# Optimization experiments

Hardware: AMD Instinct MI355X
Metric: run time of the kernel (lower is better)

## Reference

```python
import jax, jax.numpy as jnp
import numpy as np

BN_EPS = 1e-5
LN_EPS = 1e-5


def setup_inputs() -> dict:
    key = jax.random.key(0)
    ks = jax.random.split(key, 8)
    B, D, T = 16, 96, 512  # batch, enc_in (channels), d_model (time/feature)
    H = 2 * T
    residual = jax.random.normal(ks[0], (B, D, T), dtype=jnp.float32)
    # BatchNorm1d(enc_in) affine params
    bn_gamma = jnp.ones((D,), dtype=jnp.float32)
    bn_beta = jnp.zeros((D,), dtype=jnp.float32)
    # LayerNorm(d_model) affine params
    ln_gamma = jnp.ones((T,), dtype=jnp.float32)
    ln_beta = jnp.zeros((T,), dtype=jnp.float32)
    # MLP: Linear(T, 2T) -> GELU -> Linear(2T, T)
    W1 = jax.random.normal(ks[1], (T, H), dtype=jnp.float32) / np.float32(np.sqrt(T))
    b1 = jnp.zeros((H,), dtype=jnp.float32)
    W2 = jax.random.normal(ks[2], (H, T), dtype=jnp.float32) / np.float32(np.sqrt(H))
    b2 = jnp.zeros((T,), dtype=jnp.float32)
    return {"residual": residual, "bn_gamma": bn_gamma, "bn_beta": bn_beta,
            "ln_gamma": ln_gamma, "ln_beta": ln_beta,
            "W1": W1, "b1": b1, "W2": W2, "b2": b2}


def _var_cor_attention(x):
    # x: [B, D, T]; queries = keys = values = x
    B, D, T = x.shape
    f = jnp.fft.rfft(x, axis=-1)                       # [B, D, F]
    # pairwise spectral product q_i * conj(k_j): [B, D, D, F]
    res = f[:, :, None, :] * jnp.conj(f[:, None, :, :])
    corr = jnp.fft.irfft(res, axis=-1).mean(axis=-1)   # [B, D, D]
    scale = np.float32(1.0 / np.sqrt(T))
    corr = jax.nn.softmax(corr * scale, axis=-1)
    V = jnp.einsum('bsd,bde->bse', corr, x)            # [B, D, T]
    return V


def reference(residual, bn_gamma, bn_beta, ln_gamma, ln_beta, W1, b1, W2, b2):
    # attention + residual
    x = _var_cor_attention(residual) + residual        # [B, D, T]
    # BatchNorm1d over channel dim D: stats over (B, T), biased variance
    mu = x.mean(axis=(0, 2), keepdims=True)
    var = ((x - mu) ** 2).mean(axis=(0, 2), keepdims=True)
    x = (x - mu) * jax.lax.rsqrt(var + BN_EPS)
    x = x * bn_gamma[None, :, None] + bn_beta[None, :, None]
    # MLP (exact GELU, torch default) + residual
    h = jax.nn.gelu(jnp.einsum('bdt,th->bdh', x, W1) + b1, approximate=False)
    y = jnp.einsum('bdh,ht->bdt', h, W2) + b2 + x
    # LayerNorm over last dim T
    mu2 = y.mean(axis=-1, keepdims=True)
    var2 = ((y - mu2) ** 2).mean(axis=-1, keepdims=True)
    y = (y - mu2) * jax.lax.rsqrt(var2 + LN_EPS)
    return y * ln_gamma + ln_beta
```

## Files before the change

kernel.cpp:

```cpp
#include <hip/hip_runtime.h>
#include <math.h>
#include <stdint.h>

#define BB 16
#define DD 96
#define TT 512
#define HH 1024
#define NROW (BB*DD)
#define KT2 (HH/32)

typedef __attribute__((ext_vector_type(4))) float floatx4;
typedef __attribute__((ext_vector_type(8))) short short8;

#define WSOFF_X     0u
#define WSOFF_HFRAG 3145728u
#define WSOFF_W1BF  6291456u
#define WSOFF_W2BF  7340032u
#define WSOFF_PS    8388608u
#define WSOFF_PS2   8437760u
#define WSOFF_S     8486912u

__device__ __forceinline__ uint16_t f2bf(float v) {
    uint32_t u = __float_as_uint(v);
    uint32_t r = 0x7fffu + ((u >> 16) & 1u);
    return (uint16_t)((u + r) >> 16);
}

__global__ __launch_bounds__(256) void k_pre(const float* __restrict__ residual,
                                             const float* __restrict__ W1,
                                             const float* __restrict__ W2,
                                             float* __restrict__ s,
                                             uint16_t* __restrict__ w1bf,
                                             uint16_t* __restrict__ w2bf) {
    const int bid = blockIdx.x;
    const int tid = threadIdx.x;
    const int wave = tid >> 6;
    const int lane = tid & 63;
    const int q = lane >> 4, l15 = lane & 15;

    if (bid < 96) {
        int row0 = bid*16 + wave*4;
        float acc[4] = {0.f, 0.f, 0.f, 0.f};
        #pragma unroll
        for (int cc = 0; cc < 4; ++cc) {
            const float* p = residual + (size_t)(row0 + cc)*TT;
            #pragma unroll
            for (int u = 0; u < TT/64; ++u) acc[cc] += p[lane + u*64];
        }
        #pragma unroll
        for (int o = 32; o > 0; o >>= 1) {
            #pragma unroll
            for (int cc = 0; cc < 4; ++cc) acc[cc] += __shfl_down(acc[cc], o, 64);
        }
        if (lane == 0) {
            #pragma unroll
            for (int cc = 0; cc < 4; ++cc) s[row0 + cc] = acc[cc];
        }
    } else {
        int wgid = (bid - 96)*4 + wave;
        const int nw = (512 - 96)*4;
        for (int u = wgid; u < 2048; u += nw) {
            const float* W; uint16_t* ob; int KT, N, b;
            if (u < 1024) { W = W1; ob = w1bf; KT = 16; N = 1024; b = u; }
            else          { W = W2; ob = w2bf; KT = 32; N = 512;  b = u - 1024; }
            int tile_n = b / KT, tile_k = b % KT;
            const float* src = W + (size_t)(tile_k*32 + q*8)*N + tile_n*16 + l15;
            uint16_t tmp[8];
            #pragma unroll
            for (int j = 0; j < 8; ++j) tmp[j] = f2bf(src[(size_t)j*N]);
            uint16_t* dst = ob + ((size_t)b*64 + lane)*8;
            *reinterpret_cast<ushort4*>(dst)     = *reinterpret_cast<ushort4*>(&tmp[0]);
            *reinterpret_cast<ushort4*>(dst + 4) = *reinterpret_cast<ushort4*>(&tmp[4]);
        }
    }
}

__global__ __launch_bounds__(256) void k_attn(const float* __restrict__ residual,
                                              const float* __restrict__ s,
                                              float* __restrict__ x,
                                              float* __restrict__ ps,
                                              float* __restrict__ ps2) {
    __shared__ float rlds[DD*64];
    __shared__ float slds[DD];
    __shared__ float aLDS[24*DD];
    const int u = blockIdx.x;
    const int b = u >> 5, chunk = (u >> 2) & 7, ig = u & 3;
    const int tid = threadIdx.x;
    const int wave = tid >> 6;
    const int lane = tid & 63;

    const float4* rb4 = reinterpret_cast<const float4*>(residual + (size_t)b*DD*TT);
    float4* rl4 = reinterpret_cast<float4*>(rlds);
    #pragma unroll
    for (int sx = 0; sx < 6; ++sx) {
        int idx = tid + sx*256;
        int i = idx >> 4, t4 = idx & 15;
        rl4[idx] = rb4[(size_t)i*(TT/4) + chunk*16 + t4];
    }
    if (tid < DD) slds[tid] = s[b*DD + tid];
    __syncthreads();

    const float c = 1.0f / (512.0f * 22.627416997969522f);
    float sj_lo = slds[lane];
    float sj_hi = (lane < 32) ? slds[64 + lane] : 0.f;
    #pragma unroll
    for (int rr = 0; rr < 6; ++rr) {
        int iloc = wave*6 + rr;
        float si = slds[ig*24 + iloc] * c;
        float v1 = si * sj_lo;
        float v2 = (lane < 32) ? si * sj_hi : -1e30f;
        float m = fmaxf(v1, v2);
        #pragma unroll
        for (int o = 1; o < 64; o <<= 1) m = fmaxf(m, __shfl_xor(m, o, 64));
        float p1 = __expf(v1 - m);
        float p2 = (lane < 32) ? __expf(v2 - m) : 0.f;
        float sum = p1 + p2;
        #pragma unroll
        for (int o = 1; o < 64; o <<= 1) sum += __shfl_xor(sum, o, 64);
        float inv = 1.0f / sum;
        aLDS[iloc*DD + lane] = p1 * inv;
        if (lane < 32) aLDS[iloc*DD + 64 + lane] = p2 * inv;
    }

    int i0 = ig*24 + wave*6;
    float acc[6];
    #pragma unroll
    for (int rr = 0; rr < 6; ++rr) acc[rr] = rlds[(i0+rr)*64 + lane];
    #pragma unroll 4
    for (int j4 = 0; j4 < DD/4; ++j4) {
        float4 a[6];
        #pragma unroll
        for (int rr = 0; rr < 6; ++rr)
            a[rr] = *reinterpret_cast<const float4*>(&aLDS[(wave*6+rr)*DD + j4*4]);
        float rv[4];
        #pragma unroll
        for (int uu = 0; uu < 4; ++uu) rv[uu] = rlds[(j4*4+uu)*64 + lane];
        #pragma unroll
        for (int rr = 0; rr < 6; ++rr) {
            acc[rr] = fmaf(a[rr].x, rv[0], acc[rr]);
            acc[rr] = fmaf(a[rr].y, rv[1], acc[rr]);
            acc[rr] = fmaf(a[rr].z, rv[2], acc[rr]);
            acc[rr] = fmaf(a[rr].w, rv[3], acc[rr]);
        }
    }
    #pragma unroll
    for (int rr = 0; rr < 6; ++rr) {
        float v = acc[rr];
        x[((size_t)b*DD + i0 + rr)*TT + chunk*64 + lane] = v;
        float s1 = v, s2 = v*v;
        #pragma unroll
        for (int o = 32; o > 0; o >>= 1) {
            s1 += __shfl_down(s1, o, 64);
            s2 += __shfl_down(s2, o, 64);
        }
        if (lane == 0) {
            int d = i0 + rr;
            ps [d*128 + b*8 + chunk] = s1;
            ps2[d*128 + b*8 + chunk] = s2;
        }
    }
}

__device__ __forceinline__ void bn_finalize16(const float* __restrict__ ps,
                                              const float* __restrict__ ps2,
                                              const float* __restrict__ bng,
                                              const float* __restrict__ bnb,
                                              int m0, int tid, float* scs) {
    if (tid < 256) {
        int dg = tid >> 4, uu = tid & 15;
        int d = (m0 + dg) % DD;
        const float4* p1 = reinterpret_cast<const float4*>(ps  + d*128 + uu*8);
        const float4* p2 = reinterpret_cast<const float4*>(ps2 + d*128 + uu*8);
        float4 a0 = p1[0], a1 = p1[1];
        float4 b0 = p2[0], b1 = p2[1];
        float s1 = a0.x+a0.y+a0.z+a0.w + a1.x+a1.y+a1.z+a1.w;
        float s2 = b0.x+b0.y+b0.z+b0.w + b1.x+b1.y+b1.z+b1.w;
        #pragma unroll
        for (int o = 1; o < 16; o <<= 1) {
            s1 += __shfl_xor(s1, o, 16);
            s2 += __shfl_xor(s2, o, 16);
        }
        if (uu == 0) {
            const float invn = 1.0f / (float)(BB*TT);
            float mu  = s1 * invn;
            float var = s2 * invn - mu*mu;
            float rs  = rsqrtf(var + 1e-5f);
            float scv = rs * bng[d];
            scs[dg*2]     = scv;
            scs[dg*2 + 1] = bnb[d] - mu*scv;
        }
    }
}

__global__ __launch_bounds__(256) void k_gemm1(const float* __restrict__ x,
                                               const float* __restrict__ ps,
                                               const float* __restrict__ ps2,
                                               const float* __restrict__ bng,
                                               const float* __restrict__ bnb,
                                               const uint16_t* __restrict__ w1bf,
                                               const float* __restrict__ b1,
                                               uint16_t* __restrict__ hfrag) {
    __shared__ __align__(16) uint16_t fragA[16*64*8];
    __shared__ __align__(16) uint16_t cs[16][136];
    __shared__ float scs[32];
    const int mtile = blockIdx.x;
    const int m0 = mtile*16;
    const int tid = threadIdx.x;
    const int wave = tid >> 6;
    const int lane = tid & 63;
    const int q = lane >> 4, l15 = lane & 15;

    bn_finalize16(ps, ps2, bng, bnb, m0, tid, scs);
    __syncthreads();

    #pragma unroll
    for (int r4 = 0; r4 < 4; ++r4) {
        int pi = tid + r4*256;
        int kk = pi >> 6, pl = pi & 63;
        int pq = pl >> 4, pr = pl & 15;
        float scv = scs[pr*2], shv = scs[pr*2 + 1];
        const float* xp = x + (size_t)(m0 + pr)*TT + kk*32 + pq*8;
        float4 v0 = *reinterpret_cast<const float4*>(xp);
        float4 v1 = *reinterpret_cast<const float4*>(xp + 4);
        ushort4 o0, o1;
        o0.x = f2bf(v0.x*scv + shv); o0.y = f2bf(v0.y*scv + shv);
        o0.z = f2bf(v0.z*scv + shv); o0.w = f2bf(v0.w*scv + shv);
        o1.x = f2bf(v1.x*scv + shv); o1.y = f2bf(v1.y*scv + shv);
        o1.z = f2bf(v1.z*scv + shv); o1.w = f2bf(v1.w*scv + shv);
        uint16_t* fp = fragA + ((size_t)kk*64 + pl)*8;
        *reinterpret_cast<ushort4*>(fp)     = o0;
        *reinterpret_cast<ushort4*>(fp + 4) = o1;
    }
    __syncthreads();

    const int n0 = blockIdx.y*128 + wave*32;
    floatx4 acc4[2] = {};
    const uint16_t* b0p = w1bf + ((size_t)((n0>>4)    )*16*64 + lane)*8;
    const uint16_t* b1p = w1bf + ((size_t)((n0>>4) + 1)*16*64 + lane)*8;
    #pragma unroll
    for (int kk = 0; kk < 16; ++kk) {
        short8 a  = *reinterpret_cast<const short8*>(fragA + (kk*64 + lane)*8);
        short8 bb0 = *reinterpret_cast<const short8*>(b0p + kk*512);
        short8 bb1 = *reinterpret_cast<const short8*>(b1p + kk*512);
        acc4[0] = __builtin_amdgcn_mfma_f32_16x16x32_bf16(a, bb0, acc4[0], 0, 0, 0);
        acc4[1] = __builtin_amdgcn_mfma_f32_16x16x32_bf16(a, bb1, acc4[1], 0, 0, 0);
    }
    #pragma unroll
    for (int nf = 0; nf < 2; ++nf) {
        int coll = wave*32 + nf*16 + l15;
        float bias = b1[blockIdx.y*128 + coll];
        #pragma unroll
        for (int r = 0; r < 4; ++r) {
            float v = acc4[nf][r] + bias;
            float gl = 0.5f * v * (1.0f + erff(v * 0.7071067811865475f));
            cs[q*4 + r][coll] = f2bf(gl);
        }
    }
    __syncthreads();
    {
        int cchunk = wave;
        const uint4* srcp = reinterpret_cast<const uint4*>(&cs[l15][cchunk*32 + q*8]);
        size_t chunk = (size_t)mtile*KT2 + (blockIdx.y*4 + cchunk);
        reinterpret_cast<uint4*>(hfrag)[chunk*64 + lane] = *srcp;
    }
}

__global__ __launch_bounds__(256) void k_gemm2(const uint16_t* __restrict__ hfrag,
                                               const uint16_t* __restrict__ w2bf,
                                               const float* __restrict__ b2,
                                               const float* __restrict__ x,
                                               const float* __restrict__ ps,
                                               const float* __restrict__ ps2,
                                               const float* __restrict__ bng,
                                               const float* __restrict__ bnb,
                                               float* __restrict__ y) {
    __shared__ float scs[32];
    const int mtile = blockIdx.x;
    const int m0 = mtile*16;
    const int tid = threadIdx.x;
    const int wave = tid >> 6;
    const int lane = tid & 63;
    const int q = lane >> 4, l15 = lane & 15;
    const int n0 = blockIdx.y*128 + wave*32;

    bn_finalize16(ps, ps2, bng, bnb, m0, tid, scs);
    __syncthreads();

    floatx4 acc[2] = {};
    const uint16_t* ap  = hfrag + ((size_t)mtile*KT2*64 + lane)*8;
    const uint16_t* b0p = w2bf + ((size_t)((n0>>4)    )*32*64 + lane)*8;
    const uint16_t* b1p = w2bf + ((size_t)((n0>>4) + 1)*32*64 + lane)*8;
    #pragma unroll
    for (int kk = 0; kk < 32; ++kk) {
        short8 a  = *reinterpret_cast<const short8*>(ap  + kk*512);
        short8 bb0 = *reinterpret_cast<const short8*>(b0p + kk*512);
        short8 bb1 = *reinterpret_cast<const short8*>(b1p + kk*512);
        acc[0] = __builtin_amdgcn_mfma_f32_16x16x32_bf16(a, bb0, acc[0], 0, 0, 0);
        acc[1] = __builtin_amdgcn_mfma_f32_16x16x32_bf16(a, bb1, acc[1], 0, 0, 0);
    }
    #pragma unroll
    for (int nf = 0; nf < 2; ++nf) {
        int col = n0 + nf*16 + l15;
        float bias = b2[col];
        #pragma unroll
        for (int r = 0; r < 4; ++r) {
            int rloc = q*4 + r;
            int row = m0 + rloc;
            float xb = x[(size_t)row*TT + col]*scs[rloc*2] + scs[rloc*2 + 1];
            y[(size_t)row*TT + col] = acc[nf][r] + bias + xb;
        }
    }
}

__global__ __launch_bounds__(64) void k_ln(float* __restrict__ y,
                                           const float* __restrict__ lng,
                                           const float* __restrict__ lnb) {
    int row = blockIdx.x;
    int lane = threadIdx.x;
    float4* p = reinterpret_cast<float4*>(y + (size_t)row*TT);
    float4 v0 = p[lane*2], v1 = p[lane*2 + 1];
    float s  = v0.x+v0.y+v0.z+v0.w + v1.x+v1.y+v1.z+v1.w;
    float s2 = v0.x*v0.x+v0.y*v0.y+v0.z*v0.z+v0.w*v0.w
             + v1.x*v1.x+v1.y*v1.y+v1.z*v1.z+v1.w*v1.w;
    #pragma unroll
    for (int o = 1; o < 64; o <<= 1) {
        s  += __shfl_xor(s,  o, 64);
        s2 += __shfl_xor(s2, o, 64);
    }
    float mu = s * (1.0f/TT);
    float var = s2 * (1.0f/TT) - mu*mu;
    float rs = rsqrtf(var + 1e-5f);
    const float4* g4 = reinterpret_cast<const float4*>(lng);
    const float4* b4 = reinterpret_cast<const float4*>(lnb);
    float4 g0 = g4[lane*2], g1 = g4[lane*2+1];
    float4 bb0 = b4[lane*2], bb1 = b4[lane*2+1];
    float4 o0, o1;
    o0.x = (v0.x-mu)*rs*g0.x + bb0.x;  o0.y = (v0.y-mu)*rs*g0.y + bb0.y;
    o0.z = (v0.z-mu)*rs*g0.z + bb0.z;  o0.w = (v0.w-mu)*rs*g0.w + bb0.w;
    o1.x = (v1.x-mu)*rs*g1.x + bb1.x;  o1.y = (v1.y-mu)*rs*g1.y + bb1.y;
    o1.z = (v1.z-mu)*rs*g1.z + bb1.z;  o1.w = (v1.w-mu)*rs*g1.w + bb1.w;
    p[lane*2] = o0;  p[lane*2+1] = o1;
}

extern "C" void kernel_launch(void* const* d_in, const int* in_sizes, int n_in,
                              void* d_out, int out_size, void* d_ws, size_t ws_size,
                              hipStream_t stream) {
    (void)in_sizes; (void)n_in; (void)out_size; (void)ws_size;
    const float* residual = (const float*)d_in[0];
    const float* bng = (const float*)d_in[1];
    const float* bnb = (const float*)d_in[2];
    const float* lng = (const float*)d_in[3];
    const float* lnb = (const float*)d_in[4];
    const float* W1  = (const float*)d_in[5];
    const float* b1  = (const float*)d_in[6];
    const float* W2  = (const float*)d_in[7];
    const float* b2  = (const float*)d_in[8];
    float* out = (float*)d_out;
    char* ws = (char*)d_ws;
    float*    x     = (float*)(ws + WSOFF_X);
    uint16_t* hfrag = (uint16_t*)(ws + WSOFF_HFRAG);
    uint16_t* w1bf  = (uint16_t*)(ws + WSOFF_W1BF);
    uint16_t* w2bf  = (uint16_t*)(ws + WSOFF_W2BF);
    float*    ps    = (float*)(ws + WSOFF_PS);
    float*    ps2   = (float*)(ws + WSOFF_PS2);
    float*    s     = (float*)(ws + WSOFF_S);

    k_pre  <<<512, 256, 0, stream>>>(residual, W1, W2, s, w1bf, w2bf);
    k_attn <<<512, 256, 0, stream>>>(residual, s, x, ps, ps2);
    k_gemm1<<<dim3(96, 8), 256, 0, stream>>>(x, ps, ps2, bng, bnb, w1bf, b1, hfrag);
    k_gemm2<<<dim3(96, 4), 256, 0, stream>>>(hfrag, w2bf, b2, x, ps, ps2, bng, bnb, out);
    k_ln   <<<NROW, 64, 0, stream>>>(out, lng, lnb);
}
```

Measured before the change: 112.1 us.

## Process two M-tiles per block in both GEMMs and batch four LayerNorm rows per block

Each GEMM block now covers 32 rows (two 16-row M-tiles) instead of 16, so every loaded W1/W2 fragment feeds two MFMAs and weight traffic per output is halved. The grids shrink from 96 to 48 blocks in x, and the BN finalize step is reworked to compute 32 channel scales using 8 threads per channel. The LayerNorm kernel runs four rows per 256-thread block instead of one row per 64-thread block, which cuts the block count. In exchange there are fewer blocks to fill the GPU (384 and 192 for the two GEMMs), which may lower occupancy and latency hiding.

```diff
diff --git a/kernel.cpp b/kernel.cpp
--- a/kernel.cpp
+++ b/kernel.cpp
@@ -161,34 +161,34 @@
     }
 }
 
-__device__ __forceinline__ void bn_finalize16(const float* __restrict__ ps,
+__device__ __forceinline__ void bn_finalize32(const float* __restrict__ ps,
                                               const float* __restrict__ ps2,
                                               const float* __restrict__ bng,
                                               const float* __restrict__ bnb,
                                               int m0, int tid, float* scs) {
-    if (tid < 256) {
-        int dg = tid >> 4, uu = tid & 15;
-        int d = (m0 + dg) % DD;
-        const float4* p1 = reinterpret_cast<const float4*>(ps  + d*128 + uu*8);
-        const float4* p2 = reinterpret_cast<const float4*>(ps2 + d*128 + uu*8);
-        float4 a0 = p1[0], a1 = p1[1];
-        float4 b0 = p2[0], b1 = p2[1];
-        float s1 = a0.x+a0.y+a0.z+a0.w + a1.x+a1.y+a1.z+a1.w;
-        float s2 = b0.x+b0.y+b0.z+b0.w + b1.x+b1.y+b1.z+b1.w;
-        #pragma unroll
-        for (int o = 1; o < 16; o <<= 1) {
-            s1 += __shfl_xor(s1, o, 16);
-            s2 += __shfl_xor(s2, o, 16);
-        }
-        if (uu == 0) {
-            const float invn = 1.0f / (float)(BB*TT);
-            float mu  = s1 * invn;
-            float var = s2 * invn - mu*mu;
-            float rs  = rsqrtf(var + 1e-5f);
-            float scv = rs * bng[d];
-            scs[dg*2]     = scv;
-            scs[dg*2 + 1] = bnb[d] - mu*scv;
-        }
+    int dg = tid >> 3, uu = tid & 7;
+    int d = (m0 % DD) + dg;
+    const float4* p1 = reinterpret_cast<const float4*>(ps  + d*128 + uu*16);
+    const float4* p2 = reinterpret_cast<const float4*>(ps2 + d*128 + uu*16);
+    float s1 = 0.f, s2 = 0.f;
+    #pragma unroll
+    for (int j = 0; j < 4; ++j) {
+        float4 a = p1[j]; s1 += a.x+a.y+a.z+a.w;
+        float4 b = p2[j]; s2 += b.x+b.y+b.z+b.w;
+    }
+    #pragma unroll
+    for (int o = 1; o < 8; o <<= 1) {
+        s1 += __shfl_xor(s1, o, 8);
+        s2 += __shfl_xor(s2, o, 8);
+    }
+    if (uu == 0) {
+        const float invn = 1.0f / (float)(BB*TT);
+        float mu  = s1 * invn;
+        float var = s2 * invn - mu*mu;
+        float rs  = rsqrtf(var + 1e-5f);
+        float scv = rs * bng[d];
+        scs[dg*2]     = scv;
+        scs[dg*2 + 1] = bnb[d] - mu*scv;
     }
 }
 
@@ -200,26 +200,29 @@
                                                const uint16_t* __restrict__ w1bf,
                                                const float* __restrict__ b1,
                                                uint16_t* __restrict__ hfrag) {
-    __shared__ __align__(16) uint16_t fragA[16*64*8];
-    __shared__ __align__(16) uint16_t cs[16][136];
-    __shared__ float scs[32];
-    const int mtile = blockIdx.x;
-    const int m0 = mtile*16;
+    __shared__ __align__(16) uint16_t fragA[2][16*64*8];
+    __shared__ __align__(16) uint16_t cs[32][136];
+    __shared__ float scs[64];
+    const int mt0 = blockIdx.x*2;
+    const int m0 = mt0*16;
     const int tid = threadIdx.x;
     const int wave = tid >> 6;
     const int lane = tid & 63;
     const int q = lane >> 4, l15 = lane & 15;
 
-    bn_finalize16(ps, ps2, bng, bnb, m0, tid, scs);
-    __syncthreads();
-
-    #pragma unroll
-    for (int r4 = 0; r4 < 4; ++r4) {
+    bn_finalize32(ps, ps2, bng, bnb, m0, tid, scs);
+    __syncthreads();
+
+    #pragma unroll
+    for (int r4 = 0; r4 < 8; ++r4) {
         int pi = tid + r4*256;
-        int kk = pi >> 6, pl = pi & 63;
+        int mi = pi >> 10;
+        int rem = pi & 1023;
+        int kk = rem >> 6, pl = rem & 63;
         int pq = pl >> 4, pr = pl & 15;
-        float scv = scs[pr*2], shv = scs[pr*2 + 1];
-        const float* xp = x + (size_t)(m0 + pr)*TT + kk*32 + pq*8;
+        int rloc = mi*16 + pr;
+        float scv = scs[rloc*2], shv = scs[rloc*2 + 1];
+        const float* xp = x + (size_t)(m0 + rloc)*TT + kk*32 + pq*8;
         float4 v0 = *reinterpret_cast<const float4*>(xp);
         float4 v1 = *reinterpret_cast<const float4*>(xp + 4);
         ushort4 o0, o1;
@@ -227,40 +230,48 @@
         o0.z = f2bf(v0.z*scv + shv); o0.w = f2bf(v0.w*scv + shv);
         o1.x = f2bf(v1.x*scv + shv); o1.y = f2bf(v1.y*scv + shv);
         o1.z = f2bf(v1.z*scv + shv); o1.w = f2bf(v1.w*scv + shv);
-        uint16_t* fp = fragA + ((size_t)kk*64 + pl)*8;
+        uint16_t* fp = fragA[mi] + ((size_t)kk*64 + pl)*8;
         *reinterpret_cast<ushort4*>(fp)     = o0;
         *reinterpret_cast<ushort4*>(fp + 4) = o1;
     }
     __syncthreads();
 
     const int n0 = blockIdx.y*128 + wave*32;
-    floatx4 acc4[2] = {};
+    floatx4 acc4[2][2] = {};
     const uint16_t* b0p = w1bf + ((size_t)((n0>>4)    )*16*64 + lane)*8;
     const uint16_t* b1p = w1bf + ((size_t)((n0>>4) + 1)*16*64 + lane)*8;
     #pragma unroll
     for (int kk = 0; kk < 16; ++kk) {
-        short8 a  = *reinterpret_cast<const short8*>(fragA + (kk*64 + lane)*8);
         short8 bb0 = *reinterpret_cast<const short8*>(b0p + kk*512);
         short8 bb1 = *reinterpret_cast<const short8*>(b1p + kk*512);
-        acc4[0] = __builtin_amdgcn_mfma_f32_16x16x32_bf16(a, bb0, acc4[0], 0, 0, 0);
-        acc4[1] = __builtin_amdgcn_mfma_f32_16x16x32_bf16(a, bb1, acc4[1], 0, 0, 0);
-    }
-    #pragma unroll
-    for (int nf = 0; nf < 2; ++nf) {
-        int coll = wave*32 + nf*16 + l15;
-        float bias = b1[blockIdx.y*128 + coll];
-        #pragma unroll
-        for (int r = 0; r < 4; ++r) {
-            float v = acc4[nf][r] + bias;
-            float gl = 0.5f * v * (1.0f + erff(v * 0.7071067811865475f));
-            cs[q*4 + r][coll] = f2bf(gl);
-        }
-    }
-    __syncthreads();
-    {
-        int cchunk = wave;
-        const uint4* srcp = reinterpret_cast<const uint4*>(&cs[l15][cchunk*32 + q*8]);
-        size_t chunk = (size_t)mtile*KT2 + (blockIdx.y*4 + cchunk);
+        short8 a0  = *reinterpret_cast<const short8*>(fragA[0] + (kk*64 + lane)*8);
+        short8 a1  = *reinterpret_cast<const short8*>(fragA[1] + (kk*64 + lane)*8);
+        acc4[0][0] = __builtin_amdgcn_mfma_f32_16x16x32_bf16(a0, bb0, acc4[0][0], 0, 0, 0);
+        acc4[0][1] = __builtin_amdgcn_mfma_f32_16x16x32_bf16(a0, bb1, acc4[0][1], 0, 0, 0);
+        acc4[1][0] = __builtin_amdgcn_mfma_f32_16x16x32_bf16(a1, bb0, acc4[1][0], 0, 0, 0);
+        acc4[1][1] = __builtin_amdgcn_mfma_f32_16x16x32_bf16(a1, bb1, acc4[1][1], 0, 0, 0);
+    }
+    #pragma unroll
+    for (int mi = 0; mi < 2; ++mi) {
+        #pragma unroll
+        for (int nf = 0; nf < 2; ++nf) {
+            int coll = wave*32 + nf*16 + l15;
+            float bias = b1[blockIdx.y*128 + coll];
+            #pragma unroll
+            for (int r = 0; r < 4; ++r) {
+                float v = acc4[mi][nf][r] + bias;
+                float gl = 0.5f * v * (1.0f + erff(v * 0.7071067811865475f));
+                cs[mi*16 + q*4 + r][coll] = f2bf(gl);
+            }
+        }
+    }
+    __syncthreads();
+    #pragma unroll
+    for (int cc = 0; cc < 2; ++cc) {
+        int idx = wave*2 + cc;
+        int mi = idx >> 2, c = idx & 3;
+        const uint4* srcp = reinterpret_cast<const uint4*>(&cs[mi*16 + l15][c*32 + q*8]);
+        size_t chunk = (size_t)(mt0 + mi)*KT2 + (blockIdx.y*4 + c);
         reinterpret_cast<uint4*>(hfrag)[chunk*64 + lane] = *srcp;
     }
 }
@@ -274,49 +285,57 @@
                                                const float* __restrict__ bng,
                                                const float* __restrict__ bnb,
                                                float* __restrict__ y) {
-    __shared__ float scs[32];
-    const int mtile = blockIdx.x;
-    const int m0 = mtile*16;
+    __shared__ float scs[64];
+    const int mt0 = blockIdx.x*2;
+    const int m0 = mt0*16;
     const int tid = threadIdx.x;
     const int wave = tid >> 6;
     const int lane = tid & 63;
     const int q = lane >> 4, l15 = lane & 15;
     const int n0 = blockIdx.y*128 + wave*32;
 
-    bn_finalize16(ps, ps2, bng, bnb, m0, tid, scs);
-    __syncthreads();
-
-    floatx4 acc[2] = {};
-    const uint16_t* ap  = hfrag + ((size_t)mtile*KT2*64 + lane)*8;
+    bn_finalize32(ps, ps2, bng, bnb, m0, tid, scs);
+    __syncthreads();
+
+    floatx4 acc[2][2] = {};
+    const uint16_t* a0p = hfrag + ((size_t)mt0*KT2*64 + lane)*8;
+    const uint16_t* a1p = hfrag + ((size_t)(mt0 + 1)*KT2*64 + lane)*8;
     const uint16_t* b0p = w2bf + ((size_t)((n0>>4)    )*32*64 + lane)*8;
     const uint16_t* b1p = w2bf + ((size_t)((n0>>4) + 1)*32*64 + lane)*8;
     #pragma unroll
     for (int kk = 0; kk < 32; ++kk) {
-        short8 a  = *reinterpret_cast<const short8*>(ap  + kk*512);
         short8 bb0 = *reinterpret_cast<const short8*>(b0p + kk*512);
         short8 bb1 = *reinterpret_cast<const short8*>(b1p + kk*512);
-        acc[0] = __builtin_amdgcn_mfma_f32_16x16x32_bf16(a, bb0, acc[0], 0, 0, 0);
-        acc[1] = __builtin_amdgcn_mfma_f32_16x16x32_bf16(a, bb1, acc[1], 0, 0, 0);
-    }
-    #pragma unroll
-    for (int nf = 0; nf < 2; ++nf) {
-        int col = n0 + nf*16 + l15;
-        float bias = b2[col];
-        #pragma unroll
-        for (int r = 0; r < 4; ++r) {
-            int rloc = q*4 + r;
-            int row = m0 + rloc;
-            float xb = x[(size_t)row*TT + col]*scs[rloc*2] + scs[rloc*2 + 1];
-            y[(size_t)row*TT + col] = acc[nf][r] + bias + xb;
-        }
-    }
-}
-
-__global__ __launch_bounds__(64) void k_ln(float* __restrict__ y,
-                                           const float* __restrict__ lng,
-                                           const float* __restrict__ lnb) {
-    int row = blockIdx.x;
-    int lane = threadIdx.x;
+        short8 a0  = *reinterpret_cast<const short8*>(a0p + kk*512);
+        short8 a1  = *reinterpret_cast<const short8*>(a1p + kk*512);
+        acc[0][0] = __builtin_amdgcn_mfma_f32_16x16x32_bf16(a0, bb0, acc[0][0], 0, 0, 0);
+        acc[0][1] = __builtin_amdgcn_mfma_f32_16x16x32_bf16(a0, bb1, acc[0][1], 0, 0, 0);
+        acc[1][0] = __builtin_amdgcn_mfma_f32_16x16x32_bf16(a1, bb0, acc[1][0], 0, 0, 0);
+        acc[1][1] = __builtin_amdgcn_mfma_f32_16x16x32_bf16(a1, bb1, acc[1][1], 0, 0, 0);
+    }
+    #pragma unroll
+    for (int mi = 0; mi < 2; ++mi) {
+        #pragma unroll
+        for (int nf = 0; nf < 2; ++nf) {
+            int col = n0 + nf*16 + l15;
+            float bias = b2[col];
+            #pragma unroll
+            for (int r = 0; r < 4; ++r) {
+                int rloc = mi*16 + q*4 + r;
+                int row = m0 + rloc;
+                float xb = x[(size_t)row*TT + col]*scs[rloc*2] + scs[rloc*2 + 1];
+                y[(size_t)row*TT + col] = acc[mi][nf][r] + bias + xb;
+            }
+        }
+    }
+}
+
+__global__ __launch_bounds__(256) void k_ln(float* __restrict__ y,
+                                            const float* __restrict__ lng,
+                                            const float* __restrict__ lnb) {
+    int wave = threadIdx.x >> 6;
+    int lane = threadIdx.x & 63;
+    int row = blockIdx.x*4 + wave;
     float4* p = reinterpret_cast<float4*>(y + (size_t)row*TT);
     float4 v0 = p[lane*2], v1 = p[lane*2 + 1];
     float s  = v0.x+v0.y+v0.z+v0.w + v1.x+v1.y+v1.z+v1.w;
@@ -367,7 +386,7 @@
 
     k_pre  <<<512, 256, 0, stream>>>(residual, W1, W2, s, w1bf, w2bf);
     k_attn <<<512, 256, 0, stream>>>(residual, s, x, ps, ps2);
-    k_gemm1<<<dim3(96, 8), 256, 0, stream>>>(x, ps, ps2, bng, bnb, w1bf, b1, hfrag);
-    k_gemm2<<<dim3(96, 4), 256, 0, stream>>>(hfrag, w2bf, b2, x, ps, ps2, bng, bnb, out);
-    k_ln   <<<NROW, 64, 0, stream>>>(out, lng, lnb);
-}
+    k_gemm1<<<dim3(48, 8), 256, 0, stream>>>(x, ps, ps2, bng, bnb, w1bf, b1, hfrag);
+    k_gemm2<<<dim3(48, 4), 256, 0, stream>>>(hfrag, w2bf, b2, x, ps, ps2, bng, bnb, out);
+    k_ln   <<<384, 256, 0, stream>>>(out, lng, lnb);
+}
```

After: 113.9 us. About the same (+1.6%).
